# Kernel optimization log

Measured on AMD Instinct MI355X. Metric: run time of the kernel, lower is better.

The kernel has to match this reference:

```python
import jax, jax.numpy as jnp
import numpy as np
import math

B, T, D, H = 8, 1024, 512, 8
DK = D // H


def setup_inputs() -> dict:
    key = jax.random.key(0)
    ks = jax.random.split(key, 16)
    s = 1.0 / math.sqrt(D)
    inp = {
        "query": jax.random.normal(ks[0], (B, T, D), jnp.float32),
        "key": jax.random.normal(ks[1], (B, T, D), jnp.float32),
        "value": jax.random.normal(ks[2], (B, T, D), jnp.float32),
        "inputs_attn_mask": jnp.ones((B, T, T), jnp.int32),
        "pos_embed": jax.random.normal(ks[3], (B, T, D), jnp.float32),
        "Wq": jax.random.normal(ks[4], (D, D), jnp.float32) * s,
        "bq": jnp.zeros((D,), jnp.float32),
        "Wk": jax.random.normal(ks[5], (D, D), jnp.float32) * s,
        "bk": jnp.zeros((D,), jnp.float32),
        "Wv": jax.random.normal(ks[6], (D, D), jnp.float32) * s,
        "bv": jnp.zeros((D,), jnp.float32),
        "Wpos": jax.random.normal(ks[7], (D, D), jnp.float32) * s,
        "Wout": jax.random.normal(ks[8], (D, D), jnp.float32) * s,
        "bout": jnp.zeros((D,), jnp.float32),
        "pos_bias_u": jax.random.normal(ks[9], (H, DK), jnp.float32) * 0.1,
        "pos_bias_v": jax.random.normal(ks[10], (H, DK), jnp.float32) * 0.1,
    }
    return inp


def reference(query, key, value, inputs_attn_mask, pos_embed,
              Wq, bq, Wk, bk, Wv, bv, Wpos, Wout, bout,
              pos_bias_u, pos_bias_v):
    b = query.shape[0]
    # projections (torch Linear: x @ W.T + b)
    q = (query @ Wq.T + bq).reshape(b, -1, H, DK)            # [B,T,H,dk]
    k = (key @ Wk.T + bk).reshape(b, -1, H, DK).transpose(0, 2, 1, 3)   # [B,H,T,dk]
    v = (value @ Wv.T + bv).reshape(b, -1, H, DK).transpose(0, 2, 1, 3)  # [B,H,T,dk]
    new_cache = jnp.concatenate((k, v), axis=-1)             # [B,H,T,2dk]
    p = (pos_embed @ Wpos.T).reshape(b, -1, H, DK).transpose(0, 2, 1, 3)  # [B,H,T,dk]

    q_u = (q + pos_bias_u).transpose(0, 2, 1, 3)             # [B,H,T,dk]
    q_v = (q + pos_bias_v).transpose(0, 2, 1, 3)             # [B,H,T,dk]

    matrix_ac = jnp.einsum('bhtd,bhsd->bhts', q_u, k)
    matrix_bd = jnp.einsum('bhtd,bhsd->bhts', q_v, p)
    scores = (matrix_ac + matrix_bd) / math.sqrt(DK)         # [B,H,T,T]

    mask = (inputs_attn_mask[:, None, :, :] == 0)            # [B,1,T,T]
    scores = jnp.where(mask, -jnp.inf, scores)
    attn = jax.nn.softmax(scores, axis=-1)
    attn = jnp.where(mask, 0.0, attn)

    out = jnp.einsum('bhts,bhsd->bthd', attn, v).reshape(b, -1, H * DK)
    out = out @ Wout.T + bout
    return (out, new_cache)
```

## Files before the change

### kernel.cpp

```cpp
#include <hip/hip_runtime.h>

typedef __attribute__((ext_vector_type(8))) short bf16x8;
typedef __attribute__((ext_vector_type(4))) float f32x4;
typedef __attribute__((ext_vector_type(16))) float f32x16;
typedef __attribute__((ext_vector_type(4))) unsigned int u32x4;
typedef __attribute__((ext_vector_type(4))) unsigned short u16x4;

#define DEVFN static __device__ __forceinline__

DEVFN unsigned cvtpk(float lo, float hi) {
  unsigned r;
  asm("v_cvt_pk_bf16_f32 %0, %1, %2" : "=v"(r) : "v"(lo), "v"(hi));
  return r;
}
DEVFN unsigned short cvt1(float x) {
  unsigned r;
  asm("v_cvt_pk_bf16_f32 %0, %1, %1" : "=v"(r) : "v"(x));
  return (unsigned short)r;
}
DEVFN float fexp2(float x) {
  float r;
  asm("v_exp_f32 %0, %1" : "=v"(r) : "v"(x));
  return r;
}
DEVFN float bf2f(unsigned short s) { return __uint_as_float(((unsigned)s) << 16); }

DEVFN void gld16(const void* g, void* l) {
  __builtin_amdgcn_global_load_lds(
      (const __attribute__((address_space(1))) unsigned int*)g,
      (__attribute__((address_space(3))) unsigned int*)l, 16, 0, 0);
}

__global__ __launch_bounds__(256, 8) void prep_cast(
    const float* __restrict__ s0, const float* __restrict__ s1,
    const float* __restrict__ s2, const float* __restrict__ s3,
    unsigned short* __restrict__ dst, int perMat) {
  const float* s = blockIdx.y == 0 ? s0 : blockIdx.y == 1 ? s1
                   : blockIdx.y == 2 ? s2 : s3;
  size_t base = (size_t)blockIdx.y * perMat;
  size_t idx = ((size_t)blockIdx.x * 256 + threadIdx.x) * 8;
  float4 a = *(const float4*)(s + idx);
  float4 b = *(const float4*)(s + idx + 4);
  uint4 o;
  o.x = cvtpk(a.x, a.y); o.y = cvtpk(a.z, a.w);
  o.z = cvtpk(b.x, b.y); o.w = cvtpk(b.z, b.w);
  *(uint4*)(dst + base + idx) = o;
}

template <bool AF32, bool SWZ>
__global__ __launch_bounds__(256, 3) void gemm_bt(
    const void* A0, const void* A1, const void* A2, const void* A3,
    const unsigned short* __restrict__ Wb, const float* b0, const float* b1,
    const float* b2, int mode_base,
    unsigned short* __restrict__ qout, float* __restrict__ cache,
    unsigned short* __restrict__ vtout, unsigned short* __restrict__ pout,
    float* __restrict__ fout) {
  __shared__ alignas(16) char Als[128 * 128];
  __shared__ alignas(16) char Bls[2][128 * 128];
  const int tid = threadIdx.x;
  const int lane = tid & 63, w = tid >> 6;
  const int wr = (w >> 1) * 64, wc = (w & 1) * 64;
  const int lg = lane >> 4, lr = lane & 15;
  int m0, n0, mz;
  if constexpr (SWZ) {
    int id = blockIdx.x;
    int xcd = id & 7, j = id >> 3;
    n0 = (j & 3) * 128;
    mz = (j >> 2) & 3;
    m0 = (xcd * 8 + (j >> 4)) * 128;
  } else {
    m0 = blockIdx.x * 128;
    n0 = blockIdx.y * 128;
    mz = 0;
  }
  const int mode = mode_base + mz;
  const void* Ap = (mode == 1) ? A1 : (mode == 2) ? A2 : (mode == 3) ? A3 : A0;
  const unsigned short* Wp = Wb + (size_t)mz * 262144;
  const float* bias = (mode == 0 || mode == 4) ? b0
                      : (mode == 1) ? b1 : (mode == 2) ? b2 : nullptr;

  float4 ra[8];
  auto loadA = [&](int k0) {
    const float* Af = (const float*)Ap;
#pragma unroll
    for (int rep = 0; rep < 4; rep++) {
      int cid = rep * 256 + tid;
      int row = cid >> 3, c = cid & 7;
      const float* src = Af + (size_t)(m0 + row) * 512 + k0 + c * 8;
      ra[rep * 2] = *(const float4*)(src);
      ra[rep * 2 + 1] = *(const float4*)(src + 4);
    }
  };
  auto writeA = [&]() {
#pragma unroll
    for (int rep = 0; rep < 4; rep++) {
      int cid = rep * 256 + tid;
      int row = cid >> 3, c = cid & 7;
      uint4 o;
      o.x = cvtpk(ra[rep * 2].x, ra[rep * 2].y);
      o.y = cvtpk(ra[rep * 2].z, ra[rep * 2].w);
      o.z = cvtpk(ra[rep * 2 + 1].x, ra[rep * 2 + 1].y);
      o.w = cvtpk(ra[rep * 2 + 1].z, ra[rep * 2 + 1].w);
      *(uint4*)(Als + row * 128 + ((c ^ (row & 7)) << 4)) = o;
    }
  };
  auto stageA_lds = [&](int k0) {
    const unsigned short* Ab = (const unsigned short*)Ap;
#pragma unroll
    for (int rep = 0; rep < 4; rep++) {
      int cid = rep * 256 + tid;
      int row = cid >> 3, c = cid & 7;
      gld16(Ab + (size_t)(m0 + row) * 512 + k0 + ((c ^ (row & 7)) << 3),
            Als + ((rep * 256 + (w << 6)) << 4));
    }
  };
  auto stageB = [&](int buf, int k0) {
#pragma unroll
    for (int rep = 0; rep < 4; rep++) {
      int cid = rep * 256 + tid;
      int row = cid >> 3, c = cid & 7;
      gld16(Wp + (size_t)(n0 + row) * 512 + k0 + ((c ^ (row & 7)) << 3),
            Bls[buf] + ((rep * 256 + (w << 6)) << 4));
    }
  };

  f32x4 acc[4][4];
#pragma unroll
  for (int i = 0; i < 4; i++)
#pragma unroll
    for (int j = 0; j < 4; j++) acc[i][j] = (f32x4)(0.f);

  if constexpr (AF32) { loadA(0); writeA(); } else { stageA_lds(0); }
  stageB(0, 0);
  __syncthreads();
  int cur = 0;
  for (int k0 = 0; k0 < 512; k0 += 64) {
    bool more = (k0 + 64 < 512);
    if (more) {
      if constexpr (AF32) loadA(k0 + 64);
      stageB(cur ^ 1, k0 + 64);
    }
#pragma unroll
    for (int ks = 0; ks < 2; ks++) {
      bf16x8 af[4], bfr[4];
#pragma unroll
      for (int i = 0; i < 4; i++) {
        int row = wr + i * 16 + lr;
        af[i] = *(const bf16x8*)(Als + row * 128 + (((ks * 4 + lg) ^ (row & 7)) << 4));
      }
#pragma unroll
      for (int j = 0; j < 4; j++) {
        int row = wc + j * 16 + lr;
        bfr[j] = *(const bf16x8*)(Bls[cur] + row * 128 + (((ks * 4 + lg) ^ (row & 7)) << 4));
      }
#pragma unroll
      for (int i = 0; i < 4; i++)
#pragma unroll
        for (int j = 0; j < 4; j++)
          acc[i][j] = __builtin_amdgcn_mfma_f32_16x16x32_bf16(af[i], bfr[j],
                                                              acc[i][j], 0, 0, 0);
    }
    if (more) {
      __syncthreads();
      if constexpr (AF32) writeA(); else stageA_lds(k0 + 64);
      __syncthreads();
      cur ^= 1;
    }
  }

#pragma unroll
  for (int i = 0; i < 4; i++) {
#pragma unroll
    for (int j = 0; j < 4; j++) {
      int colg = n0 + wc + j * 16 + lr;
      float bc = bias ? bias[colg] : 0.f;
      if (mode == 4) {
#pragma unroll
        for (int r = 0; r < 4; r++) {
          int rowg = m0 + wr + i * 16 + lg * 4 + r;
          fout[(size_t)rowg * 512 + colg] = acc[i][j][r] + bc;
        }
      } else {
        int rbase = m0 + wr + i * 16 + lg * 4;
        int b = rbase >> 10, t = rbase & 1023, h = colg >> 6, dk = colg & 63;
        size_t bht = (size_t)(b * 8 + h) * 1024 + t;
        if (mode == 0) {
#pragma unroll
          for (int r = 0; r < 4; r++) qout[(bht + r) * 64 + dk] = cvt1(acc[i][j][r] + bc);
        } else if (mode == 1) {
#pragma unroll
          for (int r = 0; r < 4; r++) cache[(bht + r) * 128 + dk] = acc[i][j][r] + bc;
        } else if (mode == 3) {
#pragma unroll
          for (int r = 0; r < 4; r++) pout[(bht + r) * 64 + dk] = cvt1(acc[i][j][r]);
        } else {
          float vv[4];
#pragma unroll
          for (int r = 0; r < 4; r++) {
            vv[r] = acc[i][j][r] + bc;
            cache[(bht + r) * 128 + 64 + dk] = vv[r];
          }
          uint2 pv;
          pv.x = cvtpk(vv[0], vv[1]);
          pv.y = cvtpk(vv[2], vv[3]);
          *(uint2*)(vtout + ((size_t)(b * 8 + h) * 64 + dk) * 1024 + t) = pv;
        }
      }
    }
  }
}

__global__ __launch_bounds__(256, 4) void fuse_kp(
    const float* __restrict__ kcache, unsigned short* __restrict__ kp,
    const float* __restrict__ ub, const float* __restrict__ vb,
    float* __restrict__ cb) {
  int tid = threadIdx.x;
  int row = blockIdx.x * 16 + (tid >> 4);
  int g = tid & 15;
  int h = (row >> 10) & 7;
  float4 k4 = *(const float4*)(kcache + (size_t)row * 128 + g * 4);
  u16x4 p4 = *(const u16x4*)(kp + (size_t)row * 64 + g * 4);
  float4 uu = *(const float4*)(ub + h * 64 + g * 4);
  float4 vv = *(const float4*)(vb + h * 64 + g * 4);
  float kf[4] = {k4.x, k4.y, k4.z, k4.w};
  float uf[4] = {uu.x, uu.y, uu.z, uu.w};
  float vf[4] = {vv.x, vv.y, vv.z, vv.w};
  float part = 0.f;
  float s[4];
#pragma unroll
  for (int j = 0; j < 4; j++) {
    float pf = bf2f((unsigned short)p4[j]);
    s[j] = kf[j] + pf;
    part += uf[j] * kf[j] + vf[j] * pf;
  }
  uint2 o;
  o.x = cvtpk(s[0], s[1]);
  o.y = cvtpk(s[2], s[3]);
  *(uint2*)(kp + (size_t)row * 64 + g * 4) = o;
#pragma unroll
  for (int sft = 1; sft < 16; sft <<= 1) part += __shfl_xor(part, sft, 64);
  if (g == 0) cb[row] = part;
}

__global__ __launch_bounds__(256, 8) void pack_mask(
    const int* __restrict__ m, unsigned long long* __restrict__ mb) {
  int word = blockIdx.x * 4 + (threadIdx.x >> 6);
  int lane = threadIdx.x & 63;
  int v = m[(size_t)(word >> 4) * 1024 + (word & 15) * 64 + lane];
  unsigned long long bal = __ballot(v != 0);
  if (lane == 0) mb[word] = bal;
}

__global__ __launch_bounds__(256, 2) void attn_kernel(
    const unsigned short* __restrict__ qw, const unsigned short* __restrict__ kpw,
    const unsigned short* __restrict__ vtw, const float* __restrict__ cb,
    const unsigned long long* __restrict__ mbits, unsigned short* __restrict__ ow) {
  __shared__ alignas(16) char KPls[2][128 * 128];
  __shared__ alignas(16) char VTls[2][64 * 256];
  __shared__ alignas(16) float cvLS[1024];
  __shared__ alignas(16) float lsLS[4][32];

  const int tid = threadIdx.x;
  const int lane = tid & 63, w = tid >> 6;
  const int hi = lane >> 5, q5 = lane & 31;
  const int l = blockIdx.x;
  const int bh = (l & 7) * 8 + ((l >> 3) >> 3);
  const int t0 = ((l >> 3) & 7) * 128;
  const int b = bh >> 3;
  const int h = bh & 7;
  const float NEG = -3.0e38f;
  const float SC = 0.125f * 1.44269504088896f;
  const float MREF = 24.0f;

#pragma unroll
  for (int i = 0; i < 4; i++)
    cvLS[i * 256 + tid] = cb[(size_t)bh * 1024 + i * 256 + tid] * SC - MREF;

  const int qg = t0 + w * 32 + q5;
  const size_t qrow = (size_t)bh * 1024 + qg;
  bf16x8 qf[4];
#pragma unroll
  for (int ks = 0; ks < 4; ks++)
    qf[ks] = *(const bf16x8*)(qw + qrow * 64 + ks * 16 + hi * 8);

  bool wave_full;
  {
    unsigned long long accm = ~0ull;
#pragma unroll
    for (int j = 0; j < 8; j++)
      accm &= mbits[((size_t)b * 1024 + qg) * 16 + hi * 8 + j];
    wave_full = __all(accm == ~0ull);
  }

  f32x16 oacc[2];
#pragma unroll
  for (int dt = 0; dt < 2; dt++) oacc[dt] = (f32x16)(0.f);
  float mrow = 0.f, lsum = 0.f;

  auto stage = [&](int buf, int s0) {
    const size_t kr0 = (size_t)bh * 1024 + s0;
#pragma unroll
    for (int p = 0; p < 4; p++) {
      int row = p * 32 + (tid >> 3), c = tid & 7;
      gld16(kpw + (kr0 + row) * 64 + ((c ^ (row & 7)) << 3),
            KPls[buf] + p * 4096 + w * 1024);
    }
#pragma unroll
    for (int p = 0; p < 4; p++) {
      int row = p * 16 + (tid >> 4), c = tid & 15;
      gld16(vtw + ((size_t)bh * 64 + row) * 1024 + s0 + ((c ^ (row & 15)) << 3),
            VTls[buf] + p * 4096 + w * 1024);
    }
  };

  stage(0, 0);
  __syncthreads();
  int cur = 0;
  for (int it = 0; it < 8; ++it) {
    const int s0 = it * 128;
    if (it < 7) stage(cur ^ 1, s0 + 128);

#pragma unroll
    for (int t = 0; t < 4; t++) {
      f32x16 sacc = (f32x16)(0.f);
      const int arow = t * 32 + q5;
      __builtin_amdgcn_s_setprio(1);
#pragma unroll
      for (int ks = 0; ks < 4; ks++) {
        bf16x8 kf = *(const bf16x8*)(KPls[cur] + arow * 128 +
                                     (((ks * 2 + hi) ^ (arow & 7)) << 4));
        sacc = __builtin_amdgcn_mfma_f32_32x32x16_bf16(kf, qf[ks], sacc, 0, 0, 0);
      }
      __builtin_amdgcn_s_setprio(0);

      float p[16];
      if (wave_full) {
        float ls = 0.f;
#pragma unroll
        for (int rb = 0; rb < 4; rb++) {
          f32x4 cv4 = *(const f32x4*)(cvLS + s0 + t * 32 + rb * 8 + hi * 4);
#pragma unroll
          for (int j = 0; j < 4; j++) {
            int reg = rb * 4 + j;
            p[reg] = fexp2(fmaf(sacc[reg], SC, cv4[j]));
            ls += p[reg];
          }
        }
        lsum += ls;
      } else {
        unsigned long long mw =
            mbits[((size_t)b * 1024 + qg) * 16 + ((s0 + t * 32) >> 6)];
        const int bbase = (t & 1) * 32;
        float s_[16];
        float mx = NEG;
#pragma unroll
        for (int rb = 0; rb < 4; rb++) {
          f32x4 cv4 = *(const f32x4*)(cvLS + s0 + t * 32 + rb * 8 + hi * 4);
#pragma unroll
          for (int j = 0; j < 4; j++) {
            int reg = rb * 4 + j;
            s_[reg] = fmaf(sacc[reg], SC, cv4[j]);
            if ((mw >> (bbase + rb * 8 + hi * 4 + j)) & 1ull)
              mx = fmaxf(mx, s_[reg]);
          }
        }
        mx = fmaxf(mx, __shfl_xor(mx, 32, 64));
        float mn = fmaxf(mrow, mx);
        float sc = (mn == mrow) ? 1.f : fexp2(mrow - mn);
        mrow = mn;
        lsum *= sc;
#pragma unroll
        for (int rb = 0; rb < 4; rb++)
#pragma unroll
          for (int j = 0; j < 4; j++) {
            int reg = rb * 4 + j;
            bool on = (mw >> (bbase + rb * 8 + hi * 4 + j)) & 1ull;
            p[reg] = on ? fexp2(s_[reg] - mn) : 0.f;
            lsum += p[reg];
          }
        if (lane < 32) lsLS[w][q5] = sc;
        asm volatile("s_waitcnt lgkmcnt(0)" ::: "memory");
        __builtin_amdgcn_sched_barrier(0);
#pragma unroll
        for (int rb = 0; rb < 4; rb++) {
          f32x4 s4 = *(const f32x4*)(&lsLS[w][rb * 8 + hi * 4]);
#pragma unroll
          for (int j = 0; j < 4; j++) {
#pragma unroll
            for (int dt = 0; dt < 2; dt++) oacc[dt][rb * 4 + j] *= s4[j];
          }
        }
      }

#pragma unroll
      for (int ks16 = 0; ks16 < 2; ks16++) {
        unsigned a0 = cvtpk(p[ks16 * 8 + 0], p[ks16 * 8 + 1]);
        unsigned a1 = cvtpk(p[ks16 * 8 + 2], p[ks16 * 8 + 3]);
        unsigned b0 = cvtpk(p[ks16 * 8 + 4], p[ks16 * 8 + 5]);
        unsigned b1 = cvtpk(p[ks16 * 8 + 6], p[ks16 * 8 + 7]);
        unsigned xa0 = __shfl_xor(a0, 32, 64);
        unsigned xa1 = __shfl_xor(a1, 32, 64);
        unsigned xb0 = __shfl_xor(b0, 32, 64);
        unsigned xb1 = __shfl_xor(b1, 32, 64);
        u32x4 pk4;
        pk4.x = hi ? xb0 : a0;
        pk4.y = hi ? xb1 : a1;
        pk4.z = hi ? b0 : xa0;
        pk4.w = hi ? b1 : xa1;
        bf16x8 af = __builtin_bit_cast(bf16x8, pk4);
        __builtin_amdgcn_s_setprio(1);
#pragma unroll
        for (int dt = 0; dt < 2; dt++) {
          int vrow = dt * 32 + q5;
          int vc = t * 4 + ks16 * 2 + hi;
          bf16x8 vf = *(const bf16x8*)(VTls[cur] + vrow * 256 +
                                       ((vc ^ (vrow & 15)) << 4));
          oacc[dt] = __builtin_amdgcn_mfma_f32_32x32x16_bf16(af, vf, oacc[dt], 0, 0, 0);
        }
        __builtin_amdgcn_s_setprio(0);
      }
    }
    __syncthreads();
    cur ^= 1;
  }

  float tot = lsum + __shfl_xor(lsum, 32, 64);
  if (lane < 32) lsLS[w][q5] = (tot > 0.f) ? 1.f / tot : 0.f;
  asm volatile("s_waitcnt lgkmcnt(0)" ::: "memory");
  __builtin_amdgcn_sched_barrier(0);
#pragma unroll
  for (int rb = 0; rb < 4; rb++) {
    f32x4 inv4 = *(const f32x4*)(&lsLS[w][rb * 8 + hi * 4]);
#pragma unroll
    for (int j = 0; j < 4; j++) {
      int reg = rb * 4 + j;
      int qo = t0 + w * 32 + rb * 8 + hi * 4 + j;
#pragma unroll
      for (int dt = 0; dt < 2; dt++) {
        ow[((size_t)b * 1024 + qo) * 512 + h * 64 + dt * 32 + q5] =
            cvt1(oacc[dt][reg] * inv4[j]);
      }
    }
  }
}

extern "C" void kernel_launch(void* const* d_in, const int* in_sizes, int n_in,
                              void* d_out, int out_size, void* d_ws, size_t ws_size,
                              hipStream_t stream) {
  const float* query = (const float*)d_in[0];
  const float* key = (const float*)d_in[1];
  const float* value = (const float*)d_in[2];
  const int* amask = (const int*)d_in[3];
  const float* pos = (const float*)d_in[4];
  const float* Wq = (const float*)d_in[5];
  const float* bq = (const float*)d_in[6];
  const float* Wk = (const float*)d_in[7];
  const float* bk = (const float*)d_in[8];
  const float* Wv = (const float*)d_in[9];
  const float* bv = (const float*)d_in[10];
  const float* Wpos = (const float*)d_in[11];
  const float* Wout = (const float*)d_in[12];
  const float* bout = (const float*)d_in[13];
  const float* pbu = (const float*)d_in[14];
  const float* pbv = (const float*)d_in[15];

  float* out = (float*)d_out;
  float* cache = out + (size_t)8192 * 512;

  char* ws = (char*)d_ws;
  const size_t SZ = 8388608;
  dim3 blk(256);

  unsigned short* Woutb = (unsigned short*)(ws);
  unsigned short* ws_q = (unsigned short*)(ws + 4 * SZ);
  unsigned short* ws_kp = (unsigned short*)(ws + 5 * SZ);
  unsigned short* ws_vt = (unsigned short*)(ws + 6 * SZ);
  unsigned short* ws_o = (unsigned short*)(ws + 7 * SZ);
  unsigned short* W4 = ws_o;
  float* cbuf = (float*)(ws + 8 * SZ);
  unsigned long long* mbits = (unsigned long long*)(ws + 8 * SZ + 262144);

  prep_cast<<<dim3(128, 4), blk, 0, stream>>>(Wq, Wk, Wv, Wpos, W4, 262144);
  prep_cast<<<dim3(128, 1), blk, 0, stream>>>(Wout, Wout, Wout, Wout, Woutb, 262144);
  gemm_bt<true, true><<<dim3(1024), blk, 0, stream>>>(
      query, key, value, pos, W4, bq, bk, bv, 0,
      ws_q, cache, ws_vt, ws_kp, nullptr);
  fuse_kp<<<dim3(4096), blk, 0, stream>>>(cache, ws_kp, pbu, pbv, cbuf);
  pack_mask<<<dim3(32768), blk, 0, stream>>>(amask, mbits);
  attn_kernel<<<dim3(512), blk, 0, stream>>>(ws_q, ws_kp, ws_vt, cbuf, mbits, ws_o);
  gemm_bt<false, false><<<dim3(64, 4, 1), blk, 0, stream>>>(
      ws_o, nullptr, nullptr, nullptr, Woutb, bout, nullptr, nullptr, 4,
      nullptr, nullptr, nullptr, nullptr, out);
}
```

Before: 116.6 us.

## Deepen QKVP projection GEMM pipeline with double register A prefetch and manual waitcnts

Splits the templated GEMM into a dedicated QKV/pos projection kernel and an output-projection kernel. The projection kernel fully unrolls the K loop, prefetches fp32 A tiles two steps ahead into alternating register sets and stages B two buffers ahead. It replaces __syncthreads with explicit vmcnt/lgkmcnt waits, sched barriers and s_barrier so global loads can overlap MFMA work. This raises register pressure and relies on hand-counted vmcnt values being correct.

After: 141.2 us. 21.1% more time.

```diff
diff --git a/kernel.cpp b/kernel.cpp
--- a/kernel.cpp
+++ b/kernel.cpp
@@ -30,6 +30,10 @@
       (const __attribute__((address_space(1))) unsigned int*)g,
       (__attribute__((address_space(3))) unsigned int*)l, 16, 0, 0);
 }
+
+#define SFEN __builtin_amdgcn_sched_barrier(0)
+#define SBAR __builtin_amdgcn_s_barrier()
+#define LGKM0 asm volatile("s_waitcnt lgkmcnt(0)" ::: "memory")
 
 __global__ __launch_bounds__(256, 8) void prep_cast(
     const float* __restrict__ s0, const float* __restrict__ s1,
@@ -47,65 +51,172 @@
   *(uint4*)(dst + base + idx) = o;
 }
 
-template <bool AF32, bool SWZ>
-__global__ __launch_bounds__(256, 3) void gemm_bt(
-    const void* A0, const void* A1, const void* A2, const void* A3,
-    const unsigned short* __restrict__ Wb, const float* b0, const float* b1,
-    const float* b2, int mode_base,
+__global__ __launch_bounds__(256, 3) void gemm_qkvp(
+    const float* __restrict__ A0, const float* __restrict__ A1,
+    const float* __restrict__ A2, const float* __restrict__ A3,
+    const unsigned short* __restrict__ Wb, const float* __restrict__ b0,
+    const float* __restrict__ b1, const float* __restrict__ b2,
     unsigned short* __restrict__ qout, float* __restrict__ cache,
-    unsigned short* __restrict__ vtout, unsigned short* __restrict__ pout,
-    float* __restrict__ fout) {
+    unsigned short* __restrict__ vtout, unsigned short* __restrict__ pout) {
   __shared__ alignas(16) char Als[128 * 128];
   __shared__ alignas(16) char Bls[2][128 * 128];
   const int tid = threadIdx.x;
   const int lane = tid & 63, w = tid >> 6;
   const int wr = (w >> 1) * 64, wc = (w & 1) * 64;
   const int lg = lane >> 4, lr = lane & 15;
-  int m0, n0, mz;
-  if constexpr (SWZ) {
-    int id = blockIdx.x;
-    int xcd = id & 7, j = id >> 3;
-    n0 = (j & 3) * 128;
-    mz = (j >> 2) & 3;
-    m0 = (xcd * 8 + (j >> 4)) * 128;
-  } else {
-    m0 = blockIdx.x * 128;
-    n0 = blockIdx.y * 128;
-    mz = 0;
-  }
-  const int mode = mode_base + mz;
-  const void* Ap = (mode == 1) ? A1 : (mode == 2) ? A2 : (mode == 3) ? A3 : A0;
+  int id = blockIdx.x;
+  int xcd = id & 7, j = id >> 3;
+  const int n0 = (j & 3) * 128;
+  const int mz = (j >> 2) & 3;
+  const int m0 = (xcd * 8 + (j >> 4)) * 128;
+  const float* Ap = (mz == 1) ? A1 : (mz == 2) ? A2 : (mz == 3) ? A3 : A0;
   const unsigned short* Wp = Wb + (size_t)mz * 262144;
-  const float* bias = (mode == 0 || mode == 4) ? b0
-                      : (mode == 1) ? b1 : (mode == 2) ? b2 : nullptr;
-
-  float4 ra[8];
-  auto loadA = [&](int k0) {
-    const float* Af = (const float*)Ap;
+  const float* bias = (mz == 0) ? b0 : (mz == 1) ? b1 : (mz == 2) ? b2 : nullptr;
+
+  const int srow = tid >> 3, sc = tid & 7;
+
+  float4 rA[8], rB[8];
+  auto loadA = [&](float4* r, int k0) {
 #pragma unroll
     for (int rep = 0; rep < 4; rep++) {
-      int cid = rep * 256 + tid;
-      int row = cid >> 3, c = cid & 7;
-      const float* src = Af + (size_t)(m0 + row) * 512 + k0 + c * 8;
-      ra[rep * 2] = *(const float4*)(src);
-      ra[rep * 2 + 1] = *(const float4*)(src + 4);
+      int row = rep * 32 + srow;
+      const float* src = Ap + (size_t)(m0 + row) * 512 + k0 + sc * 8;
+      r[rep * 2] = *(const float4*)(src);
+      r[rep * 2 + 1] = *(const float4*)(src + 4);
     }
   };
-  auto writeA = [&]() {
+  auto writeA = [&](const float4* r) {
 #pragma unroll
     for (int rep = 0; rep < 4; rep++) {
-      int cid = rep * 256 + tid;
-      int row = cid >> 3, c = cid & 7;
+      int row = rep * 32 + srow;
       uint4 o;
-      o.x = cvtpk(ra[rep * 2].x, ra[rep * 2].y);
-      o.y = cvtpk(ra[rep * 2].z, ra[rep * 2].w);
-      o.z = cvtpk(ra[rep * 2 + 1].x, ra[rep * 2 + 1].y);
-      o.w = cvtpk(ra[rep * 2 + 1].z, ra[rep * 2 + 1].w);
-      *(uint4*)(Als + row * 128 + ((c ^ (row & 7)) << 4)) = o;
+      o.x = cvtpk(r[rep * 2].x, r[rep * 2].y);
+      o.y = cvtpk(r[rep * 2].z, r[rep * 2].w);
+      o.z = cvtpk(r[rep * 2 + 1].x, r[rep * 2 + 1].y);
+      o.w = cvtpk(r[rep * 2 + 1].z, r[rep * 2 + 1].w);
+      *(uint4*)(Als + row * 128 + ((sc ^ (row & 7)) << 4)) = o;
     }
   };
-  auto stageA_lds = [&](int k0) {
-    const unsigned short* Ab = (const unsigned short*)Ap;
+  auto stageB = [&](int buf, int k0) {
+#pragma unroll
+    for (int rep = 0; rep < 4; rep++) {
+      int row = rep * 32 + srow;
+      gld16(Wp + (size_t)(n0 + row) * 512 + k0 + ((sc ^ (row & 7)) << 3),
+            Bls[buf] + ((rep * 256 + (w << 6)) << 4));
+    }
+  };
+
+  f32x4 acc[4][4];
+#pragma unroll
+  for (int i = 0; i < 4; i++)
+#pragma unroll
+    for (int jj = 0; jj < 4; jj++) acc[i][jj] = (f32x4)(0.f);
+
+  loadA(rB, 0);
+  stageB(0, 0);
+  stageB(1, 64);
+  writeA(rB);
+  loadA(rA, 64);
+  loadA(rB, 128);
+  LGKM0;
+  SFEN;
+  asm volatile("s_waitcnt vmcnt(20)" ::: "memory");
+  SFEN;
+  SBAR;
+  SFEN;
+
+#pragma unroll
+  for (int k = 0; k < 8; k++) {
+    const int cur = k & 1;
+#pragma unroll
+    for (int ks = 0; ks < 2; ks++) {
+      bf16x8 af[4], bfr[4];
+#pragma unroll
+      for (int i = 0; i < 4; i++) {
+        int row = wr + i * 16 + lr;
+        af[i] = *(const bf16x8*)(Als + row * 128 + (((ks * 4 + lg) ^ (row & 7)) << 4));
+      }
+#pragma unroll
+      for (int jj = 0; jj < 4; jj++) {
+        int row = wc + jj * 16 + lr;
+        bfr[jj] = *(const bf16x8*)(Bls[cur] + row * 128 + (((ks * 4 + lg) ^ (row & 7)) << 4));
+      }
+#pragma unroll
+      for (int i = 0; i < 4; i++)
+#pragma unroll
+        for (int jj = 0; jj < 4; jj++)
+          acc[i][jj] = __builtin_amdgcn_mfma_f32_16x16x32_bf16(af[i], bfr[jj],
+                                                               acc[i][jj], 0, 0, 0);
+    }
+    if (k < 7) {
+      LGKM0;
+      SFEN;
+      SBAR;
+      SFEN;
+      if (k & 1) writeA(rB); else writeA(rA);
+      if (k + 3 <= 7) { if (k & 1) loadA(rB, (k + 3) * 64); else loadA(rA, (k + 3) * 64); }
+      if (k + 2 <= 7) stageB(cur, (k + 2) * 64);
+      LGKM0;
+      SFEN;
+      if (k < 5) {
+        asm volatile("s_waitcnt vmcnt(12)" ::: "memory");
+      } else if (k == 5) {
+        asm volatile("s_waitcnt vmcnt(4)" ::: "memory");
+      } else {
+        asm volatile("s_waitcnt vmcnt(0)" ::: "memory");
+      }
+      SFEN;
+      SBAR;
+      SFEN;
+    }
+  }
+
+#pragma unroll
+  for (int i = 0; i < 4; i++) {
+#pragma unroll
+    for (int jj = 0; jj < 4; jj++) {
+      int colg = n0 + wc + jj * 16 + lr;
+      float bc = bias ? bias[colg] : 0.f;
+      int rbase = m0 + wr + i * 16 + lg * 4;
+      int b = rbase >> 10, t = rbase & 1023, h = colg >> 6, dk = colg & 63;
+      size_t bht = (size_t)(b * 8 + h) * 1024 + t;
+      if (mz == 0) {
+#pragma unroll
+        for (int r = 0; r < 4; r++) qout[(bht + r) * 64 + dk] = cvt1(acc[i][jj][r] + bc);
+      } else if (mz == 1) {
+#pragma unroll
+        for (int r = 0; r < 4; r++) cache[(bht + r) * 128 + dk] = acc[i][jj][r] + bc;
+      } else if (mz == 3) {
+#pragma unroll
+        for (int r = 0; r < 4; r++) pout[(bht + r) * 64 + dk] = cvt1(acc[i][jj][r]);
+      } else {
+        float vv[4];
+#pragma unroll
+        for (int r = 0; r < 4; r++) {
+          vv[r] = acc[i][jj][r] + bc;
+          cache[(bht + r) * 128 + 64 + dk] = vv[r];
+        }
+        uint2 pv;
+        pv.x = cvtpk(vv[0], vv[1]);
+        pv.y = cvtpk(vv[2], vv[3]);
+        *(uint2*)(vtout + ((size_t)(b * 8 + h) * 64 + dk) * 1024 + t) = pv;
+      }
+    }
+  }
+}
+
+__global__ __launch_bounds__(256, 3) void gemm_out(
+    const unsigned short* __restrict__ Ab, const unsigned short* __restrict__ Wp,
+    const float* __restrict__ bias, float* __restrict__ fout) {
+  __shared__ alignas(16) char Als[128 * 128];
+  __shared__ alignas(16) char Bls[2][128 * 128];
+  const int tid = threadIdx.x;
+  const int lane = tid & 63, w = tid >> 6;
+  const int wr = (w >> 1) * 64, wc = (w & 1) * 64;
+  const int lg = lane >> 4, lr = lane & 15;
+  const int m0 = blockIdx.x * 128, n0 = blockIdx.y * 128;
+
+  auto stageA = [&](int k0) {
 #pragma unroll
     for (int rep = 0; rep < 4; rep++) {
       int cid = rep * 256 + tid;
@@ -130,16 +241,13 @@
 #pragma unroll
     for (int j = 0; j < 4; j++) acc[i][j] = (f32x4)(0.f);
 
-  if constexpr (AF32) { loadA(0); writeA(); } else { stageA_lds(0); }
+  stageA(0);
   stageB(0, 0);
   __syncthreads();
   int cur = 0;
   for (int k0 = 0; k0 < 512; k0 += 64) {
     bool more = (k0 + 64 < 512);
-    if (more) {
-      if constexpr (AF32) loadA(k0 + 64);
-      stageB(cur ^ 1, k0 + 64);
-    }
+    if (more) stageB(cur ^ 1, k0 + 64);
 #pragma unroll
     for (int ks = 0; ks < 2; ks++) {
       bf16x8 af[4], bfr[4];
@@ -162,7 +270,7 @@
     }
     if (more) {
       __syncthreads();
-      if constexpr (AF32) writeA(); else stageA_lds(k0 + 64);
+      stageA(k0 + 64);
       __syncthreads();
       cur ^= 1;
     }
@@ -173,38 +281,11 @@
 #pragma unroll
     for (int j = 0; j < 4; j++) {
       int colg = n0 + wc + j * 16 + lr;
-      float bc = bias ? bias[colg] : 0.f;
-      if (mode == 4) {
-#pragma unroll
-        for (int r = 0; r < 4; r++) {
-          int rowg = m0 + wr + i * 16 + lg * 4 + r;
-          fout[(size_t)rowg * 512 + colg] = acc[i][j][r] + bc;
-        }
-      } else {
-        int rbase = m0 + wr + i * 16 + lg * 4;
-        int b = rbase >> 10, t = rbase & 1023, h = colg >> 6, dk = colg & 63;
-        size_t bht = (size_t)(b * 8 + h) * 1024 + t;
-        if (mode == 0) {
-#pragma unroll
-          for (int r = 0; r < 4; r++) qout[(bht + r) * 64 + dk] = cvt1(acc[i][j][r] + bc);
-        } else if (mode == 1) {
-#pragma unroll
-          for (int r = 0; r < 4; r++) cache[(bht + r) * 128 + dk] = acc[i][j][r] + bc;
-        } else if (mode == 3) {
-#pragma unroll
-          for (int r = 0; r < 4; r++) pout[(bht + r) * 64 + dk] = cvt1(acc[i][j][r]);
-        } else {
-          float vv[4];
-#pragma unroll
-          for (int r = 0; r < 4; r++) {
-            vv[r] = acc[i][j][r] + bc;
-            cache[(bht + r) * 128 + 64 + dk] = vv[r];
-          }
-          uint2 pv;
-          pv.x = cvtpk(vv[0], vv[1]);
-          pv.y = cvtpk(vv[2], vv[3]);
-          *(uint2*)(vtout + ((size_t)(b * 8 + h) * 64 + dk) * 1024 + t) = pv;
-        }
+      float bc = bias[colg];
+#pragma unroll
+      for (int r = 0; r < 4; r++) {
+        int rowg = m0 + wr + i * 16 + lg * 4 + r;
+        fout[(size_t)rowg * 512 + colg] = acc[i][j][r] + bc;
       }
     }
   }
@@ -482,13 +563,10 @@
 
   prep_cast<<<dim3(128, 4), blk, 0, stream>>>(Wq, Wk, Wv, Wpos, W4, 262144);
   prep_cast<<<dim3(128, 1), blk, 0, stream>>>(Wout, Wout, Wout, Wout, Woutb, 262144);
-  gemm_bt<true, true><<<dim3(1024), blk, 0, stream>>>(
-      query, key, value, pos, W4, bq, bk, bv, 0,
-      ws_q, cache, ws_vt, ws_kp, nullptr);
+  gemm_qkvp<<<dim3(1024), blk, 0, stream>>>(
+      query, key, value, pos, W4, bq, bk, bv, ws_q, cache, ws_vt, ws_kp);
   fuse_kp<<<dim3(4096), blk, 0, stream>>>(cache, ws_kp, pbu, pbv, cbuf);
   pack_mask<<<dim3(32768), blk, 0, stream>>>(amask, mbits);
   attn_kernel<<<dim3(512), blk, 0, stream>>>(ws_q, ws_kp, ws_vt, cbuf, mbits, ws_o);
-  gemm_bt<false, false><<<dim3(64, 4, 1), blk, 0, stream>>>(
-      ws_o, nullptr, nullptr, nullptr, Woutb, bout, nullptr, nullptr, 4,
-      nullptr, nullptr, nullptr, nullptr, out);
-}
+  gemm_out<<<dim3(64, 4), blk, 0, stream>>>(ws_o, Woutb, bout, out);
+}
```
